# Kernel tuning notes

Hardware: AMD Instinct MI355X
Metric: run time of the kernel (lower is better)

## Reference

```python
import jax, jax.numpy as jnp
import numpy as np

N_HEADS = 8
DIM_HEAD = 64
SCALE = DIM_HEAD ** -0.5


def setup_inputs() -> dict:
    key = jax.random.key(0)
    ks = jax.random.split(key, 7)
    B, C, H, W = 2, 512, 64, 64
    inner = N_HEADS * DIM_HEAD  # 512
    x = jax.random.normal(ks[0], (B, C, H, W), dtype=jnp.float32)
    context = jax.random.normal(ks[1], (B, C, H, W), dtype=jnp.float32)
    # kaiming_normal fan_out for 1x1 conv: std = sqrt(2 / out_channels)
    std_qkv = (2.0 / inner) ** 0.5
    std_o = (2.0 / C) ** 0.5
    Wq = jax.random.normal(ks[2], (inner, C), dtype=jnp.float32) * std_qkv
    Wk = jax.random.normal(ks[3], (inner, C), dtype=jnp.float32) * std_qkv
    Wv = jax.random.normal(ks[4], (inner, C), dtype=jnp.float32) * std_qkv
    Wo = jax.random.normal(ks[5], (C, inner), dtype=jnp.float32) * std_o
    return {
        'x': x, 'context': context,
        'Wq': Wq, 'bq': jnp.zeros((inner,), jnp.float32),
        'Wk': Wk, 'bk': jnp.zeros((inner,), jnp.float32),
        'Wv': Wv, 'bv': jnp.zeros((inner,), jnp.float32),
        'Wo': Wo, 'bo': jnp.zeros((C,), jnp.float32),
    }


def _attention(x, context, Wq, bq, Wk, bk, Wv, bv, Wo, bo):
    b, c, h, w = x.shape
    s = h * w
    # 1x1 conv == per-pixel channel matmul. Flatten spatial: [b, s, c]
    xf = x.reshape(b, c, s).transpose(0, 2, 1)
    cf = context.reshape(b, c, s).transpose(0, 2, 1)
    q = jnp.einsum('bsc,ec->bse', xf, Wq) + bq  # [b, s, inner]
    k = jnp.einsum('bsc,ec->bse', cf, Wk) + bk
    v = jnp.einsum('bsc,ec->bse', cf, Wv) + bv
    # split heads: [b, n, s, d]
    def split(t):
        return t.reshape(b, s, N_HEADS, DIM_HEAD).transpose(0, 2, 1, 3)
    q, k, v = split(q), split(k), split(v)
    sim = jnp.einsum('bnid,bnjd->bnij', q, k) * SCALE  # [b, n, s, s]
    attn = jax.nn.softmax(sim, axis=-1)
    out = jnp.einsum('bnij,bnjd->bnid', attn, v)  # [b, n, s, d]
    # merge heads back to channels: 'b n s d -> b (n d) s'
    out = out.transpose(0, 2, 1, 3).reshape(b, s, N_HEADS * DIM_HEAD)
    out = jnp.einsum('bse,ce->bsc', out, Wo) + bo  # output proj (1x1 conv)
    return out.transpose(0, 2, 1).reshape(b, c, h, w)


def reference(x, context, Wq, bq, Wk, bk, Wv, bv, Wo, bo):
    return _attention(x, context, Wq, bq, Wk, bk, Wv, bv, Wo, bo)
```

## Files before the change

### kernel.cpp

```cpp
#include <hip/hip_runtime.h>
#include <cstdint>


typedef __bf16 bf16x8 __attribute__((ext_vector_type(8)));
typedef __bf16 bf16x4 __attribute__((ext_vector_type(4)));
typedef float f32x4 __attribute__((ext_vector_type(4)));
typedef unsigned short u16x8 __attribute__((ext_vector_type(8)));
typedef unsigned short u16x4 __attribute__((ext_vector_type(4)));

#define AS1 __attribute__((address_space(1)))
#define AS3 __attribute__((address_space(3)))

__device__ __forceinline__ void async16(const void* g, void* l) {
  __builtin_amdgcn_global_load_lds((const AS1 void*)g, (AS3 void*)l, 16, 0, 0);
}

__device__ __forceinline__ uint16_t f2bf(float f) {
  union { float f; uint32_t u; } a;
  a.f = f;
  uint32_t r = a.u + 0x7fffu + ((a.u >> 16) & 1u);
  return (uint16_t)(r >> 16);
}

__global__ __launch_bounds__(256) void cvt_w(
    const float* __restrict__ W0, const float* __restrict__ W1,
    const float* __restrict__ W2, const float* __restrict__ W3,
    uint16_t* __restrict__ O0, uint16_t* __restrict__ O1,
    uint16_t* __restrict__ O2, uint16_t* __restrict__ O3) {
  const float* W[4] = {W0, W1, W2, W3};
  uint16_t* O[4] = {O0, O1, O2, O3};
  const int w = blockIdx.y;
  const int i = (blockIdx.x * 256 + threadIdx.x) * 4;
  float4 v = *(const float4*)&W[w][i];
  u16x4 o = {f2bf(v.x), f2bf(v.y), f2bf(v.z), f2bf(v.w)};
  *(u16x4*)&O[w][i] = o;
}

__global__ __launch_bounds__(256) void transpose_cs(
    const float* __restrict__ x, const float* __restrict__ ctx,
    uint16_t* __restrict__ xT, uint16_t* __restrict__ cT) {
  const int zz = blockIdx.z;
  const float* src = (zz < 2 ? x : ctx) + (size_t)(zz & 1) * 512 * 4096;
  uint16_t* dst = (zz < 2 ? xT : cT) + (size_t)(zz & 1) * 4096 * 512;
  const int s0 = blockIdx.x * 64, c0 = blockIdx.y * 64;
  __shared__ uint16_t tile[64][80];
  const int t = threadIdx.x;
  for (int p = 0; p < 2; ++p) {
    int u = p * 256 + t;
    int r = u >> 3, cg = (u & 7) * 8;
    const float* sp = &src[(size_t)(c0 + r) * 4096 + s0 + cg];
    float4 v0 = *(const float4*)sp;
    float4 v1 = *(const float4*)(sp + 4);
    u16x8 o = {f2bf(v0.x), f2bf(v0.y), f2bf(v0.z), f2bf(v0.w),
               f2bf(v1.x), f2bf(v1.y), f2bf(v1.z), f2bf(v1.w)};
    *(u16x8*)&tile[r][cg] = o;
  }
  __syncthreads();
  for (int p = 0; p < 2; ++p) {
    int u = p * 256 + t;
    int sr = u >> 3, cg = (u & 7) * 8;
    u16x8 v;
    for (int j = 0; j < 8; ++j) v[j] = tile[cg + j][sr];
    *(u16x8*)&dst[(size_t)(s0 + sr) * 512 + c0 + cg] = v;
  }
}

struct QkvArgs {
  const uint16_t* A[3]; long long sA[3];
  const uint16_t* B[3]; long long sB[3];
  uint16_t* C[3];       long long sC[3];
  const float* bias[3];
  int N[3]; int lx[3]; int brow[3];
};

__global__ __launch_bounds__(256) void gemm_qkv(QkvArgs ga) {
  constexpr int K = 512;
  __shared__ uint16_t At[128 * 32];
  __shared__ uint16_t Bt[128 * 32];
  const int t = threadIdx.x, lane = t & 63, wave = t >> 6;
  const int lr = lane & 15, lq = lane >> 4;
  const int wm = (wave >> 1) * 64, wn = (wave & 1) * 64;
  const int sel = blockIdx.z >> 1, bat = blockIdx.z & 1;
  const int lx = ga.lx[sel], N = ga.N[sel], brow = ga.brow[sel];
  const int n0 = (blockIdx.x & ((1 << lx) - 1)) * 128;
  const int m0 = (blockIdx.x >> lx) * 128;
  const uint16_t* A = ga.A[sel] + (size_t)bat * ga.sA[sel];
  const uint16_t* B = ga.B[sel] + (size_t)bat * ga.sB[sel];
  const float* bias = ga.bias[sel];
  f32x4 acc[4][4] = {};
  for (int k0 = 0; k0 < K; k0 += 32) {
    __syncthreads();
    for (int p = 0; p < 2; ++p) {
      int u = p * 256 + t;
      int r = u >> 2, c = (u & 3) * 8;
      async16(&A[(size_t)(m0 + r) * K + k0 + c], &At[p * 2048 + wave * 512]);
      async16(&B[(size_t)(n0 + r) * K + k0 + c], &Bt[p * 2048 + wave * 512]);
    }
    __syncthreads();
    bf16x8 af[4], bfr[4];
    for (int i = 0; i < 4; ++i)
      af[i] = *(const bf16x8*)&At[(wm + i * 16 + lr) * 32 + lq * 8];
    for (int j = 0; j < 4; ++j)
      bfr[j] = *(const bf16x8*)&Bt[(wn + j * 16 + lr) * 32 + lq * 8];
    for (int i = 0; i < 4; ++i)
      for (int j = 0; j < 4; ++j)
        acc[i][j] = __builtin_amdgcn_mfma_f32_16x16x32_bf16(af[i], bfr[j], acc[i][j], 0, 0, 0);
  }
  uint16_t* C = ga.C[sel] + (size_t)bat * ga.sC[sel];
  for (int i = 0; i < 4; ++i)
    for (int j = 0; j < 4; ++j) {
      int row = m0 + wm + i * 16 + lq * 4;
      int col = n0 + wn + j * 16 + lr;
      float bc = brow ? 0.f : bias[col];
      for (int r = 0; r < 4; ++r) {
        float val = acc[i][j][r] + (brow ? bias[row + r] : bc);
        C[(size_t)(row + r) * N + col] = f2bf(val);
      }
    }
}

__global__ __launch_bounds__(256) void gemm_out(
    const uint16_t* __restrict__ Wo, const uint16_t* __restrict__ Ob,
    long long sB, float* __restrict__ Y, long long sC, int N,
    const float* __restrict__ bias) {
  constexpr int K = 512;
  __shared__ uint16_t At[128 * 32];
  __shared__ uint16_t Bt[128 * 32];
  const int t = threadIdx.x, lane = t & 63, wave = t >> 6;
  const int lr = lane & 15, lq = lane >> 4;
  const int wm = (wave >> 1) * 64, wn = (wave & 1) * 64;
  const int m0 = blockIdx.y * 128, n0 = blockIdx.x * 128;
  const uint16_t* B = Ob + (size_t)blockIdx.z * sB;
  f32x4 acc[4][4] = {};
  for (int k0 = 0; k0 < K; k0 += 32) {
    __syncthreads();
    for (int p = 0; p < 2; ++p) {
      int u = p * 256 + t;
      int r = u >> 2, c = (u & 3) * 8;
      async16(&Wo[(size_t)(m0 + r) * K + k0 + c], &At[p * 2048 + wave * 512]);
      async16(&B[(size_t)(n0 + r) * K + k0 + c], &Bt[p * 2048 + wave * 512]);
    }
    __syncthreads();
    bf16x8 af[4], bfr[4];
    for (int i = 0; i < 4; ++i)
      af[i] = *(const bf16x8*)&At[(wm + i * 16 + lr) * 32 + lq * 8];
    for (int j = 0; j < 4; ++j)
      bfr[j] = *(const bf16x8*)&Bt[(wn + j * 16 + lr) * 32 + lq * 8];
    for (int i = 0; i < 4; ++i)
      for (int j = 0; j < 4; ++j)
        acc[i][j] = __builtin_amdgcn_mfma_f32_16x16x32_bf16(af[i], bfr[j], acc[i][j], 0, 0, 0);
  }
  float* Cf = Y + (size_t)blockIdx.z * sC;
  for (int i = 0; i < 4; ++i)
    for (int j = 0; j < 4; ++j) {
      int row = m0 + wm + i * 16 + lq * 4;
      int col = n0 + wn + j * 16 + lr;
      for (int r = 0; r < 4; ++r)
        Cf[(size_t)(row + r) * N + col] = acc[i][j][r] + bias[row + r];
    }
}

__global__ __launch_bounds__(256) void attn128(
    const uint16_t* __restrict__ Q, const uint16_t* __restrict__ K,
    const uint16_t* __restrict__ Vt, uint16_t* __restrict__ O) {
  constexpr int S = 4096, E = 512;
  const int b = blockIdx.z, h = blockIdx.y;
  const int i0 = blockIdx.x * 128;
  const int t = threadIdx.x, lane = t & 63, wave = t >> 6;
  const int lr = lane & 15, lq = lane >> 4;
  const size_t qkB = (size_t)b * S * E;
  const size_t vB = (size_t)b * E * S;
  __shared__ uint16_t Kl[64 * 64];
  __shared__ uint16_t Vl[64 * 64];
  __shared__ __bf16 Pl[4 * 2 * 16 * 72];

  const int qbase = i0 + wave * 32;
  bf16x8 qf[2][2];
  for (int g = 0; g < 2; ++g) {
    const size_t qo = qkB + (size_t)(qbase + g * 16 + lr) * E + h * 64 + lq * 8;
    qf[g][0] = *(const bf16x8*)&Q[qo];
    qf[g][1] = *(const bf16x8*)&Q[qo + 32];
  }
  f32x4 lsum[2] = {};
  f32x4 accOT[2][4] = {};
  const float slh = 0.125f * 1.44269504088896f;
  const int swz = (lr & 7);

  for (int j0 = 0; j0 < S; j0 += 64) {
    __syncthreads();
    for (int p = 0; p < 2; ++p) {
      int u = p * 256 + t;
      int rr = u >> 3;
      int sc = (u & 7) ^ (rr & 7);
      async16(&K[qkB + (size_t)(j0 + rr) * E + h * 64 + sc * 8], &Kl[p * 2048 + wave * 512]);
      async16(&Vt[vB + (size_t)(h * 64 + rr) * S + j0 + sc * 8], &Vl[p * 2048 + wave * 512]);
    }
    __syncthreads();
    f32x4 svt[2][4];
    for (int jn = 0; jn < 4; ++jn) {
      const int row = jn * 16 + lr;
      const int c0 = (lq ^ swz) * 8;
      bf16x8 ka0 = *(const bf16x8*)&Kl[row * 64 + c0];
      bf16x8 ka1 = *(const bf16x8*)&Kl[row * 64 + (c0 ^ 32)];
      for (int g = 0; g < 2; ++g) {
        f32x4 z = {0.f, 0.f, 0.f, 0.f};
        z = __builtin_amdgcn_mfma_f32_16x16x32_bf16(ka0, qf[g][0], z, 0, 0, 0);
        z = __builtin_amdgcn_mfma_f32_16x16x32_bf16(ka1, qf[g][1], z, 0, 0, 0);
        svt[g][jn] = z;
      }
    }
    for (int g = 0; g < 2; ++g) {
      __bf16* pr = &Pl[((wave * 2 + g) * 16 + lr) * 72];
      for (int jn = 0; jn < 4; ++jn) {
        f32x4 p;
        for (int r = 0; r < 4; ++r) p[r] = exp2f(svt[g][jn][r] * slh);
        lsum[g] += p;
        bf16x4 pk;
        for (int r = 0; r < 4; ++r) pk[r] = (__bf16)p[r];
        *(bf16x4*)&pr[jn * 16 + lq * 4] = pk;
      }
    }
    bf16x8 pa[2][2];
    for (int g = 0; g < 2; ++g) {
      const __bf16* pr = &Pl[((wave * 2 + g) * 16 + lr) * 72];
      pa[g][0] = *(const bf16x8*)&pr[lq * 8];
      pa[g][1] = *(const bf16x8*)&pr[32 + lq * 8];
    }
    for (int dn = 0; dn < 4; ++dn) {
      const int row = dn * 16 + lr;
      const int c0 = (lq ^ swz) * 8;
      bf16x8 v0 = *(const bf16x8*)&Vl[row * 64 + c0];
      bf16x8 v1 = *(const bf16x8*)&Vl[row * 64 + (c0 ^ 32)];
      for (int g = 0; g < 2; ++g) {
        accOT[g][dn] = __builtin_amdgcn_mfma_f32_16x16x32_bf16(v0, pa[g][0], accOT[g][dn], 0, 0, 0);
        accOT[g][dn] = __builtin_amdgcn_mfma_f32_16x16x32_bf16(v1, pa[g][1], accOT[g][dn], 0, 0, 0);
      }
    }
  }
  for (int g = 0; g < 2; ++g) {
    float lt = (lsum[g][0] + lsum[g][1]) + (lsum[g][2] + lsum[g][3]);
    lt += __shfl_xor(lt, 16);
    lt += __shfl_xor(lt, 32);
    const float inv = 1.f / lt;
    const size_t row = qbase + g * 16 + lr;
    for (int dn = 0; dn < 4; ++dn) {
      u16x4 o;
      for (int r = 0; r < 4; ++r) o[r] = f2bf(accOT[g][dn][r] * inv);
      *(u16x4*)&O[qkB + row * E + h * 64 + dn * 16 + lq * 4] = o;
    }
  }
}

extern "C" void kernel_launch(void* const* d_in, const int* in_sizes, int n_in,
                              void* d_out, int out_size, void* d_ws, size_t ws_size,
                              hipStream_t stream) {
  const float* x   = (const float*)d_in[0];
  const float* ctx = (const float*)d_in[1];
  const float* Wq  = (const float*)d_in[2];
  const float* bq  = (const float*)d_in[3];
  const float* Wk  = (const float*)d_in[4];
  const float* bk  = (const float*)d_in[5];
  const float* Wv  = (const float*)d_in[6];
  const float* bv  = (const float*)d_in[7];
  const float* Wo  = (const float*)d_in[8];
  const float* bo  = (const float*)d_in[9];
  float* out = (float*)d_out;

  const size_t SZ = (size_t)2 * 4096 * 512;
  uint16_t* xT = (uint16_t*)d_ws;
  uint16_t* cT = xT + SZ;
  uint16_t* Qb = cT + SZ;
  uint16_t* Kb = Qb + SZ;
  uint16_t* Vb = Kb + SZ;
  uint16_t* Ob = Vb + SZ;
  uint16_t* Wqb = Ob + SZ;
  uint16_t* Wkb = Wqb + 512 * 512;
  uint16_t* Wvb = Wkb + 512 * 512;
  uint16_t* Wob = Wvb + 512 * 512;
  const long long sIn = 4096LL * 512LL;

  cvt_w<<<dim3(256, 4), 256, 0, stream>>>(Wq, Wk, Wv, Wo, Wqb, Wkb, Wvb, Wob);
  transpose_cs<<<dim3(64, 8, 4), 256, 0, stream>>>(x, ctx, xT, cT);
  QkvArgs qkv = {
      {xT, cT, Wvb}, {sIn, sIn, 0},
      {Wqb, Wkb, cT}, {0, 0, sIn},
      {Qb, Kb, Vb}, {sIn, sIn, sIn},
      {bq, bk, bv},
      {512, 512, 4096}, {2, 2, 5}, {0, 0, 1}};
  gemm_qkv<<<dim3(128, 1, 6), 256, 0, stream>>>(qkv);
  attn128<<<dim3(32, 8, 2), 256, 0, stream>>>(Qb, Kb, Vb, Ob);
  gemm_out<<<dim3(32, 4, 2), 256, 0, stream>>>(Wob, Ob, sIn, out, sIn, 4096, bo);
}
```

Before: 268.1 us.

## Split attention over key halves with combine kernel; halve gemm_out M tile

Attention work is split across two key-range halves, which doubles the grid from 512 to 1024 blocks so more of the GPU's compute units stay busy. Each half writes unnormalized bf16 partial outputs and row sums, and a new combine kernel adds them and normalizes. The softmax scale is folded into the Q projection epilogue, which removes a multiply in the attention inner loop. gemm_out switches to 64-row tiles to double its block count. The cost is an extra kernel launch, extra workspace traffic for the partials, and an additional bf16 rounding step on the partial outputs.

Measured after the change: 262.1 us. -2.2%, faster.

```diff
diff --git a/kernel.cpp b/kernel.cpp
--- a/kernel.cpp
+++ b/kernel.cpp
@@ -20,6 +20,12 @@
   a.f = f;
   uint32_t r = a.u + 0x7fffu + ((a.u >> 16) & 1u);
   return (uint16_t)(r >> 16);
+}
+
+__device__ __forceinline__ float bf2f(uint16_t u) {
+  union { uint32_t u; float f; } a;
+  a.u = (uint32_t)u << 16;
+  return a.f;
 }
 
 __global__ __launch_bounds__(256) void cvt_w(
@@ -70,6 +76,7 @@
   const uint16_t* B[3]; long long sB[3];
   uint16_t* C[3];       long long sC[3];
   const float* bias[3];
+  float os[3];
   int N[3]; int lx[3]; int brow[3];
 };
 
@@ -82,6 +89,7 @@
   const int wm = (wave >> 1) * 64, wn = (wave & 1) * 64;
   const int sel = blockIdx.z >> 1, bat = blockIdx.z & 1;
   const int lx = ga.lx[sel], N = ga.N[sel], brow = ga.brow[sel];
+  const float os = ga.os[sel];
   const int n0 = (blockIdx.x & ((1 << lx) - 1)) * 128;
   const int m0 = (blockIdx.x >> lx) * 128;
   const uint16_t* A = ga.A[sel] + (size_t)bat * ga.sA[sel];
@@ -113,7 +121,7 @@
       int col = n0 + wn + j * 16 + lr;
       float bc = brow ? 0.f : bias[col];
       for (int r = 0; r < 4; ++r) {
-        float val = acc[i][j][r] + (brow ? bias[row + r] : bc);
+        float val = (acc[i][j][r] + (brow ? bias[row + r] : bc)) * os;
         C[(size_t)(row + r) * N + col] = f2bf(val);
       }
     }
@@ -124,34 +132,37 @@
     long long sB, float* __restrict__ Y, long long sC, int N,
     const float* __restrict__ bias) {
   constexpr int K = 512;
-  __shared__ uint16_t At[128 * 32];
+  __shared__ uint16_t At[64 * 32];
   __shared__ uint16_t Bt[128 * 32];
   const int t = threadIdx.x, lane = t & 63, wave = t >> 6;
   const int lr = lane & 15, lq = lane >> 4;
-  const int wm = (wave >> 1) * 64, wn = (wave & 1) * 64;
-  const int m0 = blockIdx.y * 128, n0 = blockIdx.x * 128;
+  const int wm = (wave >> 1) * 32, wn = (wave & 1) * 64;
+  const int m0 = blockIdx.y * 64, n0 = blockIdx.x * 128;
   const uint16_t* B = Ob + (size_t)blockIdx.z * sB;
-  f32x4 acc[4][4] = {};
+  f32x4 acc[2][4] = {};
   for (int k0 = 0; k0 < K; k0 += 32) {
     __syncthreads();
+    {
+      int r = t >> 2, c = (t & 3) * 8;
+      async16(&Wo[(size_t)(m0 + r) * K + k0 + c], &At[wave * 512]);
+    }
     for (int p = 0; p < 2; ++p) {
       int u = p * 256 + t;
       int r = u >> 2, c = (u & 3) * 8;
-      async16(&Wo[(size_t)(m0 + r) * K + k0 + c], &At[p * 2048 + wave * 512]);
       async16(&B[(size_t)(n0 + r) * K + k0 + c], &Bt[p * 2048 + wave * 512]);
     }
     __syncthreads();
-    bf16x8 af[4], bfr[4];
-    for (int i = 0; i < 4; ++i)
+    bf16x8 af[2], bfr[4];
+    for (int i = 0; i < 2; ++i)
       af[i] = *(const bf16x8*)&At[(wm + i * 16 + lr) * 32 + lq * 8];
     for (int j = 0; j < 4; ++j)
       bfr[j] = *(const bf16x8*)&Bt[(wn + j * 16 + lr) * 32 + lq * 8];
-    for (int i = 0; i < 4; ++i)
+    for (int i = 0; i < 2; ++i)
       for (int j = 0; j < 4; ++j)
         acc[i][j] = __builtin_amdgcn_mfma_f32_16x16x32_bf16(af[i], bfr[j], acc[i][j], 0, 0, 0);
   }
   float* Cf = Y + (size_t)blockIdx.z * sC;
-  for (int i = 0; i < 4; ++i)
+  for (int i = 0; i < 2; ++i)
     for (int j = 0; j < 4; ++j) {
       int row = m0 + wm + i * 16 + lq * 4;
       int col = n0 + wn + j * 16 + lr;
@@ -162,9 +173,11 @@
 
 __global__ __launch_bounds__(256) void attn128(
     const uint16_t* __restrict__ Q, const uint16_t* __restrict__ K,
-    const uint16_t* __restrict__ Vt, uint16_t* __restrict__ O) {
+    const uint16_t* __restrict__ Vt, uint16_t* __restrict__ Ap,
+    float* __restrict__ Lp) {
   constexpr int S = 4096, E = 512;
-  const int b = blockIdx.z, h = blockIdx.y;
+  const int b = blockIdx.z & 1, jh = blockIdx.z >> 1;
+  const int h = blockIdx.y;
   const int i0 = blockIdx.x * 128;
   const int t = threadIdx.x, lane = t & 63, wave = t >> 6;
   const int lr = lane & 15, lq = lane >> 4;
@@ -183,10 +196,10 @@
   }
   f32x4 lsum[2] = {};
   f32x4 accOT[2][4] = {};
-  const float slh = 0.125f * 1.44269504088896f;
   const int swz = (lr & 7);
 
-  for (int j0 = 0; j0 < S; j0 += 64) {
+  const int jbeg = jh * (S / 2), jend = jbeg + S / 2;
+  for (int j0 = jbeg; j0 < jend; j0 += 64) {
     __syncthreads();
     for (int p = 0; p < 2; ++p) {
       int u = p * 256 + t;
@@ -213,7 +226,7 @@
       __bf16* pr = &Pl[((wave * 2 + g) * 16 + lr) * 72];
       for (int jn = 0; jn < 4; ++jn) {
         f32x4 p;
-        for (int r = 0; r < 4; ++r) p[r] = exp2f(svt[g][jn][r] * slh);
+        for (int r = 0; r < 4; ++r) p[r] = exp2f(svt[g][jn][r]);
         lsum[g] += p;
         bf16x4 pk;
         for (int r = 0; r < 4; ++r) pk[r] = (__bf16)p[r];
@@ -237,18 +250,40 @@
       }
     }
   }
+  uint16_t* Aph = Ap + (size_t)jh * 2 * S * E;
+  float* Lph = Lp + ((size_t)(jh * 2 + b) * 8 + h) * S;
   for (int g = 0; g < 2; ++g) {
     float lt = (lsum[g][0] + lsum[g][1]) + (lsum[g][2] + lsum[g][3]);
     lt += __shfl_xor(lt, 16);
     lt += __shfl_xor(lt, 32);
-    const float inv = 1.f / lt;
+    if (lane < 16) Lph[qbase + g * 16 + lr] = lt;
     const size_t row = qbase + g * 16 + lr;
     for (int dn = 0; dn < 4; ++dn) {
       u16x4 o;
-      for (int r = 0; r < 4; ++r) o[r] = f2bf(accOT[g][dn][r] * inv);
-      *(u16x4*)&O[qkB + row * E + h * 64 + dn * 16 + lq * 4] = o;
-    }
-  }
+      for (int r = 0; r < 4; ++r) o[r] = f2bf(accOT[g][dn][r]);
+      *(u16x4*)&Aph[qkB + row * E + h * 64 + dn * 16 + lq * 4] = o;
+    }
+  }
+}
+
+__global__ __launch_bounds__(256) void attn_combine(
+    const uint16_t* __restrict__ Ap, const float* __restrict__ Lp,
+    uint16_t* __restrict__ Ob) {
+  constexpr int S = 4096, E = 512;
+  const size_t HALF = (size_t)2 * S * E;
+  const size_t idx = ((size_t)blockIdx.x * 256 + threadIdx.x) * 4;
+  const int b = (int)(idx / ((size_t)S * E));
+  const size_t rem = idx % ((size_t)S * E);
+  const int s = (int)(rem / E), e = (int)(rem % E);
+  const int h = e >> 6;
+  const float l0 = Lp[((size_t)(0 * 2 + b) * 8 + h) * S + s];
+  const float l1 = Lp[((size_t)(1 * 2 + b) * 8 + h) * S + s];
+  const float inv = 1.f / (l0 + l1);
+  u16x4 a0 = *(const u16x4*)&Ap[idx];
+  u16x4 a1 = *(const u16x4*)&Ap[HALF + idx];
+  u16x4 o;
+  for (int r = 0; r < 4; ++r) o[r] = f2bf((bf2f(a0[r]) + bf2f(a1[r])) * inv);
+  *(u16x4*)&Ob[idx] = o;
 }
 
 extern "C" void kernel_launch(void* const* d_in, const int* in_sizes, int n_in,
@@ -277,7 +312,10 @@
   uint16_t* Wkb = Wqb + 512 * 512;
   uint16_t* Wvb = Wkb + 512 * 512;
   uint16_t* Wob = Wvb + 512 * 512;
+  uint16_t* Ap  = Wob + 512 * 512;
+  float*    Lp  = (float*)(Ap + 2 * SZ);
   const long long sIn = 4096LL * 512LL;
+  const float slh = 0.125f * 1.44269504088896f;
 
   cvt_w<<<dim3(256, 4), 256, 0, stream>>>(Wq, Wk, Wv, Wo, Wqb, Wkb, Wvb, Wob);
   transpose_cs<<<dim3(64, 8, 4), 256, 0, stream>>>(x, ctx, xT, cT);
@@ -286,8 +324,10 @@
       {Wqb, Wkb, cT}, {0, 0, sIn},
       {Qb, Kb, Vb}, {sIn, sIn, sIn},
       {bq, bk, bv},
+      {slh, 1.f, 1.f},
       {512, 512, 4096}, {2, 2, 5}, {0, 0, 1}};
   gemm_qkv<<<dim3(128, 1, 6), 256, 0, stream>>>(qkv);
-  attn128<<<dim3(32, 8, 2), 256, 0, stream>>>(Qb, Kb, Vb, Ob);
-  gemm_out<<<dim3(32, 4, 2), 256, 0, stream>>>(Wob, Ob, sIn, out, sIn, 4096, bo);
-}
+  attn128<<<dim3(32, 8, 4), 256, 0, stream>>>(Qb, Kb, Vb, Ap, Lp);
+  attn_combine<<<dim3(4096), 256, 0, stream>>>(Ap, Lp, Ob);
+  gemm_out<<<dim3(32, 8, 2), 256, 0, stream>>>(Wob, Ob, sIn, out, sIn, 4096, bo);
+}
```
